# Performance work log

Measured on AMD Instinct MI355X. Metric: run time of the kernel, lower is better.

Reference implementation:

```python
import jax, jax.numpy as jnp
import numpy as np

HIDDEN = 2048
N_HEADS = 32
N_KV_HEADS = 8
HEAD_DIM = 64
ROPE_THETA = 500000.0
B, S = 1, 2048


def _rope_tables(seq_len):
    inv_freq = 1.0 / ROPE_THETA ** (jnp.arange(0, HEAD_DIM, 2, dtype=jnp.float32) / HEAD_DIM)
    angles = jnp.arange(seq_len, dtype=jnp.float32)[:, None] * inv_freq[None, :]
    return jnp.cos(angles), jnp.sin(angles)


def _apply_rope(x, cos, sin):
    # x: (B, S, H, D); cos/sin: (S, D//2)
    x1 = x[..., 0::2]
    x2 = x[..., 1::2]
    c = cos[None, :, None, :]
    s = sin[None, :, None, :]
    x1r = x1 * c - x2 * s
    x2r = x1 * s + x2 * c
    return jnp.stack([x1r, x2r], axis=-1).reshape(x.shape)


def setup_inputs() -> dict:
    key = jax.random.key(0)
    ks = jax.random.split(key, 5)
    hidden_states = jax.random.normal(ks[0], (B, S, HIDDEN), dtype=jnp.float32)
    # causal mask, broadcastable over (B, H, S, S)
    attention_mask = jnp.tril(jnp.ones((S, S), dtype=bool))[None, :, :]
    sc = 1.0 / np.sqrt(HIDDEN)
    wq = jax.random.normal(ks[1], (HIDDEN, N_HEADS * HEAD_DIM), dtype=jnp.float32) * sc
    wk = jax.random.normal(ks[2], (HIDDEN, N_KV_HEADS * HEAD_DIM), dtype=jnp.float32) * sc
    wv = jax.random.normal(ks[3], (HIDDEN, N_KV_HEADS * HEAD_DIM), dtype=jnp.float32) * sc
    wo = jax.random.normal(ks[4], (N_HEADS * HEAD_DIM, HIDDEN), dtype=jnp.float32) * sc
    return {"hidden_states": hidden_states, "attention_mask": attention_mask,
            "wq": wq, "wk": wk, "wv": wv, "wo": wo}


def reference(hidden_states, attention_mask, wq, wk, wv, wo):
    b, s, _ = hidden_states.shape
    groups = N_HEADS // N_KV_HEADS
    q = (hidden_states @ wq).reshape(b, s, N_HEADS, HEAD_DIM)
    k = (hidden_states @ wk).reshape(b, s, N_KV_HEADS, HEAD_DIM)
    v = (hidden_states @ wv).reshape(b, s, N_KV_HEADS, HEAD_DIM)
    cos, sin = _rope_tables(s)
    q = _apply_rope(q, cos, sin)
    k = _apply_rope(k, cos, sin)
    k = jnp.repeat(k, groups, axis=2)  # (b, s, H, D)
    v = jnp.repeat(v, groups, axis=2)
    q = q.transpose(0, 2, 1, 3)  # (b, H, s, D)
    k = k.transpose(0, 2, 1, 3)
    v = v.transpose(0, 2, 1, 3)
    scores = jnp.einsum('bhqd,bhkd->bhqk', q, k) / jnp.sqrt(jnp.float32(HEAD_DIM))
    scores = jnp.where(attention_mask[:, None, :, :], scores, -jnp.inf)
    probs = jax.nn.softmax(scores, axis=-1)
    out = jnp.einsum('bhqk,bhkd->bhqd', probs, v)
    out = out.transpose(0, 2, 1, 3).reshape(b, s, N_HEADS * HEAD_DIM)
    return out @ wo
```

## Files before the change

kernel.cpp:

```cpp
#include <hip/hip_runtime.h>

typedef __attribute__((ext_vector_type(8))) short short8;
typedef __attribute__((ext_vector_type(4))) float float4v;

union U4S8 { uint4 u; short8 s; };

__device__ __forceinline__ float bf2f(ushort u) {
    union { uint i; float f; } v; v.i = ((uint)u) << 16; return v.f;
}
__device__ __forceinline__ ushort f2bf(float f) {
    union { uint i; float f; } v; v.f = f;
    return (ushort)((v.i + 0x7FFFu + ((v.i >> 16) & 1u)) >> 16);
}
#if __has_builtin(__builtin_amdgcn_cvt_pk_bf16_f32)
__device__ __forceinline__ uint f2bf_pk(float a, float b) {
    auto r = __builtin_amdgcn_cvt_pk_bf16_f32(a, b);
    return __builtin_bit_cast(uint, r);
}
#else
__device__ __forceinline__ uint f2bf_pk(float a, float b) {
    return (uint)f2bf(a) | ((uint)f2bf(b) << 16);
}
#endif
__device__ __forceinline__ void gld_lds16(const ushort* g, ushort* l) {
    __builtin_amdgcn_global_load_lds((const __attribute__((address_space(1))) unsigned int*)g,
                                     (__attribute__((address_space(3))) unsigned int*)l,
                                     16, 0, 0);
}

__device__ __forceinline__ void tconv_body(const float* in, ushort* out,
                                           int C, int r0, int c0, int tid) {
    __shared__ float t[64][65];
    const int lrow = tid >> 2;
    const int lc   = (tid & 3) * 16;
    const float* ip = in + (size_t)(r0 + lrow) * C + c0 + lc;
#pragma unroll
    for (int i = 0; i < 4; i++) {
        float4 v = *(const float4*)(ip + 4 * i);
        t[lrow][lc + 4 * i + 0] = v.x; t[lrow][lc + 4 * i + 1] = v.y;
        t[lrow][lc + 4 * i + 2] = v.z; t[lrow][lc + 4 * i + 3] = v.w;
    }
    __syncthreads();
    ushort* op = out + (size_t)(c0 + lrow) * 2048 + r0 + lc;
#pragma unroll
    for (int i = 0; i < 8; i++)
        ((uint*)op)[i] = f2bf_pk(t[lc + 2 * i][lrow], t[lc + 2 * i + 1][lrow]);
}

__global__ __launch_bounds__(256) void prep(const float* __restrict__ hidden,
                                            const float* __restrict__ wq,
                                            const float* __restrict__ wk,
                                            const float* __restrict__ wv,
                                            ushort* __restrict__ hid,
                                            ushort* __restrict__ wT) {
    const int bx = blockIdx.x;
    if (bx < 2048) {
        const size_t i = ((size_t)bx * 256 + threadIdx.x) * 8;
        float4 a = *(const float4*)(hidden + i);
        float4 b = *(const float4*)(hidden + i + 4);
        uint4 u;
        u.x = f2bf_pk(a.x, a.y); u.y = f2bf_pk(a.z, a.w);
        u.z = f2bf_pk(b.x, b.y); u.w = f2bf_pk(b.z, b.w);
        *(uint4*)(hid + i) = u;
    } else {
        const int i = bx - 2048;
        const int xx = i % 48, yy = i / 48;
        const float* in; ushort* op; int C, cx;
        if (xx < 32)      { in = wq; op = wT;                        C = 2048; cx = xx; }
        else if (xx < 40) { in = wk; op = wT + (size_t)2048 * 2048;  C = 512;  cx = xx - 32; }
        else              { in = wv; op = wT + (size_t)2560 * 2048;  C = 512;  cx = xx - 40; }
        tconv_body(in, op, C, yy * 64, cx * 64, threadIdx.x);
    }
}

__global__ __launch_bounds__(256) void mid(ushort* __restrict__ Qb,
                                           ushort* __restrict__ Kc,
                                           const float* __restrict__ wo,
                                           ushort* __restrict__ woT) {
    const int bx = blockIdx.x;
    if (bx < 10240) {
        const int idx = bx * 256 + threadIdx.x;
        const int QP = 2048 * 1024;
        int s, p; ushort* base; float osc;
        if (idx < QP) { s = idx >> 10; p = idx & 1023; base = Qb; osc = 0.18033688f; }
        else { int r = idx - QP; s = r >> 8; p = r & 255; base = Kc; osc = 1.0f; }
        const int j = p & 31;
        float inv = __expf(-(float)(2 * j) * (1.0f / 64.0f) * 13.122363377404328f);
        float sn, c;
        sincosf((float)s * inv, &sn, &c);
        uint* p2 = (uint*)(base + (size_t)s * 3072 + 2 * p);
        uint xv = *p2;
        float x1 = bf2f((ushort)(xv & 0xFFFFu)), x2 = bf2f((ushort)(xv >> 16));
        *p2 = f2bf_pk((x1 * c - x2 * sn) * osc, (x1 * sn + x2 * c) * osc);
    } else {
        const int i = bx - 10240;
        tconv_body(wo, woT, 2048, (i >> 5) * 64, (i & 31) * 64, threadIdx.x);
    }
}

template <bool BF16OUT>
__global__ __launch_bounds__(256) void gemm_n64(const ushort* __restrict__ A,
                                                const ushort* __restrict__ Bt,
                                                void* __restrict__ Cout,
                                                int N, int K, int lda) {
    __shared__ ushort As[2][128 * 32];
    __shared__ ushort Bs[2][64 * 32];

    const int tid = threadIdx.x, w = tid >> 6, lane = tid & 63;
    const int lr = lane & 15, quad = lane >> 4;
    const int m0 = blockIdx.x * 128, n0 = blockIdx.y * 64;

    const int srow = lane >> 2;
    const int skb  = (lane & 3) ^ ((srow >> 1) & 3);

    const ushort* Ap = A  + (size_t)(m0 + srow) * lda + skb * 8;
    const ushort* Bp = Bt + (size_t)(n0 + w * 16 + srow) * K + skb * 8;

    float4v acc[2][4];
#pragma unroll
    for (int a = 0; a < 2; a++)
#pragma unroll
        for (int b = 0; b < 4; b++) { acc[a][b][0] = 0.f; acc[a][b][1] = 0.f; acc[a][b][2] = 0.f; acc[a][b][3] = 0.f; }

    const int fsw = (lr >> 1) & 3;

#pragma unroll
    for (int i = 0; i < 2; i++) {
        const int rt = 2 * w + i;
        gld_lds16(Ap + (size_t)(rt * 16) * lda, &As[0][rt * 512]);
    }
    gld_lds16(Bp, &Bs[0][w * 512]);

    const int niter = K >> 5;
    for (int it = 0; it < niter; it++) {
        const int b = it & 1;

        asm volatile("s_waitcnt vmcnt(0) lgkmcnt(0)\n\ts_barrier" ::: "memory");

        if (it + 1 < niter) {
            const int k1 = (it + 1) << 5;
#pragma unroll
            for (int i = 0; i < 2; i++) {
                const int rt = 2 * w + i;
                gld_lds16(Ap + (size_t)(rt * 16) * lda + k1, &As[1 - b][rt * 512]);
            }
            gld_lds16(Bp + k1, &Bs[1 - b][w * 512]);
        }

        short8 af[2], bf[4];
#pragma unroll
        for (int mt = 0; mt < 2; mt++)
            af[mt] = *(const short8*)&As[b][(w * 32 + mt * 16 + lr) * 32 + (quad ^ fsw) * 8];
#pragma unroll
        for (int nt = 0; nt < 4; nt++)
            bf[nt] = *(const short8*)&Bs[b][(nt * 16 + lr) * 32 + (quad ^ fsw) * 8];
#pragma unroll
        for (int mt = 0; mt < 2; mt++)
#pragma unroll
            for (int nt = 0; nt < 4; nt++)
                acc[mt][nt] = __builtin_amdgcn_mfma_f32_16x16x32_bf16(af[mt], bf[nt], acc[mt][nt], 0, 0, 0);
    }

    const int rbase = m0 + w * 32 + quad * 4;
    const int cbase = n0 + lr;
#pragma unroll
    for (int mt = 0; mt < 2; mt++)
#pragma unroll
        for (int nt = 0; nt < 4; nt++)
#pragma unroll
            for (int r = 0; r < 4; r++) {
                const size_t idx = (size_t)(rbase + mt * 16 + r) * N + cbase + nt * 16;
                if (BF16OUT) ((ushort*)Cout)[idx] = f2bf(acc[mt][nt][r]);
                else         ((float*)Cout)[idx]  = acc[mt][nt][r];
            }
}

__global__ __launch_bounds__(256) void attn_mfma(const ushort* __restrict__ Q,
                                                 const ushort* __restrict__ Kc,
                                                 const ushort* __restrict__ Vc,
                                                 ushort* __restrict__ O0,
                                                 ushort* __restrict__ O1,
                                                 float* __restrict__ L0,
                                                 float* __restrict__ L1) {
    __shared__ ushort Ks[2][64 * 64];
    __shared__ ushort Vt[2][64 * 64];
    __shared__ ushort Ps[4][16 * 64];

    const int tid = threadIdx.x, w = tid >> 6, lane = tid & 63;
    const int lr = lane & 15, quad = lane >> 4;
    const int h = blockIdx.y, g = h >> 2, z = blockIdx.z;

    const int dg = tid & 15;
    const int kl = tid >> 4;
    const int ksub = lane >> 3, dsub = lane & 7;
    ushort* Pw = Ps[w];
    ushort* Op = z ? O1 : O0;
    float*  Lp = z ? L1 : L0;

    const ushort* Vp0 = Vc + g * 64 + dg * 4 + (size_t)3072 * kl;
    const ushort* Kp0 = Kc + g * 64 + ((dsub ^ ksub) * 8) + (size_t)3072 * ksub;

    short8 onesf;
#pragma unroll
    for (int j = 0; j < 8; j++) onesf[j] = (short)0x3F80;

    for (int ti = 0; ti < 2; ti++) {
        const int bx = ti ? 31 - (int)blockIdx.x : (int)blockIdx.x;
        const int nch = (bx >= z) ? ((bx - z) >> 1) + 1 : 0;
        const int last = z + 2 * (nch - 1);

        const ushort* qp = Q + (size_t)(bx * 64 + w * 16 + lr) * 3072 + h * 64 + quad * 8;
        const short8 qf0 = *(const short8*)qp;
        const short8 qf1 = *(const short8*)(qp + 32);

        float4v oacc[4], lacc;
#pragma unroll
        for (int t = 0; t < 4; t++) { oacc[t][0] = 0.f; oacc[t][1] = 0.f; oacc[t][2] = 0.f; oacc[t][3] = 0.f; }
        lacc[0] = 0.f; lacc[1] = 0.f; lacc[2] = 0.f; lacc[3] = 0.f;

        uint2 vv[4];
        if (nch) {
#pragma unroll
            for (int t = 0; t < 4; t++)
                vv[t] = *(const uint2*)(Vp0 + (size_t)(z * 64 + 16 * t) * 3072);
        }
        __syncthreads();
        if (nch) {
#pragma unroll
            for (int i = 0; i < 2; i++) {
                const int rt = 2 * w + i;
                gld_lds16(Kp0 + (size_t)(z * 64 + rt * 8) * 3072, &Ks[0][rt * 512]);
            }
        }

        for (int c = 0; c < nch; c++) {
            const int kb = z + 2 * c;
            const int b = c & 1;
            ushort* bKs = Ks[b];
            ushort* bVt = Vt[b];

#pragma unroll
            for (int i = 0; i < 4; i++) {
                const uint sel = (i & 1) ? 0x07060302u : 0x05040100u;
                uint s0 = (i < 2) ? vv[0].x : vv[0].y;
                uint s1 = (i < 2) ? vv[1].x : vv[1].y;
                uint s2 = (i < 2) ? vv[2].x : vv[2].y;
                uint s3 = (i < 2) ? vv[3].x : vv[3].y;
                uint2 pk;
                pk.x = __builtin_amdgcn_perm(s1, s0, sel);
                pk.y = __builtin_amdgcn_perm(s3, s2, sel);
                *(uint2*)&bVt[(dg * 4 + i) * 64 + (kl ^ ((dg & 3) * 4 + i)) * 4] = pk;
            }

            const int kn = (c + 1 < nch) ? kb + 2 : last;
#pragma unroll
            for (int t = 0; t < 4; t++)
                vv[t] = *(const uint2*)(Vp0 + (size_t)(kn * 64 + 16 * t) * 3072);

            asm volatile("s_waitcnt vmcnt(4) lgkmcnt(0)\n\ts_barrier" ::: "memory");

#pragma unroll
            for (int i = 0; i < 2; i++) {
                const int rt = 2 * w + i;
                gld_lds16(Kp0 + (size_t)(kn * 64 + rt * 8) * 3072, &Ks[1 - b][rt * 512]);
            }

            float4v sacc[4];
#pragma unroll
            for (int t = 0; t < 4; t++) { sacc[t][0] = 0.f; sacc[t][1] = 0.f; sacc[t][2] = 0.f; sacc[t][3] = 0.f; }
#pragma unroll
            for (int t = 0; t < 4; t++) {
                const int krow = t * 16 + lr;
                const int sw = lr & 7;
                short8 kf0 = *(const short8*)&bKs[krow * 64 + ((quad)     ^ sw) * 8];
                short8 kf1 = *(const short8*)&bKs[krow * 64 + ((quad + 4) ^ sw) * 8];
                sacc[t] = __builtin_amdgcn_mfma_f32_16x16x32_bf16(qf0, kf0, sacc[t], 0, 0, 0);
                sacc[t] = __builtin_amdgcn_mfma_f32_16x16x32_bf16(qf1, kf1, sacc[t], 0, 0, 0);
            }

            if (kb == bx) {
#pragma unroll
                for (int r = 0; r < 4; r++) {
                    const int qr = w * 16 + quad * 4 + r;
                    float p0 = exp2f(sacc[0][r]), p1 = exp2f(sacc[1][r]);
                    float p2 = exp2f(sacc[2][r]), p3 = exp2f(sacc[3][r]);
                    if (lr > qr)      p0 = 0.f;
                    if (16 + lr > qr) p1 = 0.f;
                    if (32 + lr > qr) p2 = 0.f;
                    if (48 + lr > qr) p3 = 0.f;
                    const int prow = quad * 4 + r;
                    uint2 pk; pk.x = f2bf_pk(p0, p1); pk.y = f2bf_pk(p2, p3);
                    *(uint2*)&Pw[prow * 64 + (lr ^ prow) * 4] = pk;
                }
            } else {
#pragma unroll
                for (int r = 0; r < 4; r++) {
                    const int prow = quad * 4 + r;
                    uint2 pk;
                    pk.x = f2bf_pk(exp2f(sacc[0][r]), exp2f(sacc[1][r]));
                    pk.y = f2bf_pk(exp2f(sacc[2][r]), exp2f(sacc[3][r]));
                    *(uint2*)&Pw[prow * 64 + (lr ^ prow) * 4] = pk;
                }
            }

#pragma unroll
            for (int ks2 = 0; ks2 < 2; ks2++) {
                const int ub = ks2 * 8 + quad * 2;
                U4S8 pu;
                uint2 plo = *(const uint2*)&Pw[lr * 64 + ((ub)     ^ lr) * 4];
                uint2 phi = *(const uint2*)&Pw[lr * 64 + ((ub + 1) ^ lr) * 4];
                pu.u.x = plo.x; pu.u.y = plo.y; pu.u.z = phi.x; pu.u.w = phi.y;
                lacc = __builtin_amdgcn_mfma_f32_16x16x32_bf16(pu.s, onesf, lacc, 0, 0, 0);
#pragma unroll
                for (int t = 0; t < 4; t++) {
                    const int d = t * 16 + lr;
                    U4S8 vu;
                    uint2 vlo = *(const uint2*)&bVt[d * 64 + ((ub)     ^ lr) * 4];
                    uint2 vhi = *(const uint2*)&bVt[d * 64 + ((ub + 1) ^ lr) * 4];
                    vu.u.x = vlo.x; vu.u.y = vlo.y; vu.u.z = vhi.x; vu.u.w = vhi.y;
                    oacc[t] = __builtin_amdgcn_mfma_f32_16x16x32_bf16(pu.s, vu.s, oacc[t], 0, 0, 0);
                }
            }
        }

        ushort* op = Op + (size_t)(bx * 64 + w * 16 + quad * 4) * 2048 + h * 64 + lr;
#pragma unroll
        for (int t = 0; t < 4; t++)
#pragma unroll
            for (int r = 0; r < 4; r++)
                op[(size_t)r * 2048 + t * 16] = f2bf(oacc[t][r]);
        if (lr == 0) {
#pragma unroll
            for (int r = 0; r < 4; r++)
                Lp[h * 2048 + bx * 64 + w * 16 + quad * 4 + r] = lacc[r];
        }
    }
}

__global__ __launch_bounds__(256) void combine(const ushort* __restrict__ O0,
                                               const ushort* __restrict__ O1,
                                               const float* __restrict__ L0,
                                               const float* __restrict__ L1,
                                               ushort* __restrict__ Ab) {
    const int idx = blockIdx.x * 256 + threadIdx.x;
    const int r = idx >> 8;
    const int c8 = (idx & 255) * 8;
    const int h = c8 >> 6;
    const float rl = 1.0f / (L0[h * 2048 + r] + L1[h * 2048 + r]);
    uint4 a = *(const uint4*)(O0 + (size_t)r * 2048 + c8);
    uint4 b = *(const uint4*)(O1 + (size_t)r * 2048 + c8);
    uint ua[4] = {a.x, a.y, a.z, a.w}, ub[4] = {b.x, b.y, b.z, b.w};
    uint4 res;
    uint rr[4];
#pragma unroll
    for (int k = 0; k < 4; k++) {
        float x0 = bf2f((ushort)(ua[k] & 0xFFFFu)) + bf2f((ushort)(ub[k] & 0xFFFFu));
        float x1 = bf2f((ushort)(ua[k] >> 16))     + bf2f((ushort)(ub[k] >> 16));
        rr[k] = f2bf_pk(x0 * rl, x1 * rl);
    }
    res.x = rr[0]; res.y = rr[1]; res.z = rr[2]; res.w = rr[3];
    *(uint4*)(Ab + (size_t)r * 3072 + c8) = res;
}

extern "C" void kernel_launch(void* const* d_in, const int* in_sizes, int n_in,
                              void* d_out, int out_size, void* d_ws, size_t ws_size,
                              hipStream_t stream) {
    const float* hidden = (const float*)d_in[0];
    const float* wq = (const float*)d_in[2];
    const float* wk = (const float*)d_in[3];
    const float* wv = (const float*)d_in[4];
    const float* wo = (const float*)d_in[5];

    ushort* ws = (ushort*)d_ws;
    ushort* hid  = ws;
    ushort* wT   = ws + 4194304;
    ushort* QKV  = ws + 10485760;
    ushort* Qb = QKV;
    ushort* Kc = QKV + 2048;
    ushort* Vc = QKV + 2560;
    ushort* O1 = (ushort*)d_out;
    float*  L0 = (float*)((ushort*)d_out + 4194304);
    float*  L1 = L0 + 65536;

    prep<<<3584, 256, 0, stream>>>(hidden, wq, wk, wv, hid, wT);
    gemm_n64<true><<<dim3(16, 48), 256, 0, stream>>>(hid, wT, QKV, 3072, 2048, 2048);
    mid<<<11264, 256, 0, stream>>>(Qb, Kc, wo, wT);
    attn_mfma<<<dim3(16, 32, 2), 256, 0, stream>>>(Qb, Kc, Vc, hid , O1, L0, L1);
    combine<<<2048, 256, 0, stream>>>(hid, O1, L0, L1, Qb );
    gemm_n64<false><<<dim3(16, 32), 256, 0, stream>>>(Qb, wT, d_out, 2048, 2048, 3072);
}
```

Measured before the change: 243.3 us.

## Split-K both projection GEMMs into two halves and fold partial sums downstream

Both GEMMs are launched with a K-split of two along blockIdx.z, doubling the block count (768→1536 and 512→1024) so more CUs have work. For the QKV GEMM the second partial is written as bf16 into the output buffer, and the mid kernel adds the two partials before applying RoPE, with a new block range handling V. For the output GEMM, z=0 writes fp32 and a new addp kernel adds the bf16 second partial. This costs extra partial-buffer traffic, one extra launch, and rounding of the partial sums to bf16.

```diff
diff --git a/kernel.cpp b/kernel.cpp
--- a/kernel.cpp
+++ b/kernel.cpp
@@ -73,48 +73,66 @@
     }
 }
 
-__global__ __launch_bounds__(256) void mid(ushort* __restrict__ Qb,
-                                           ushort* __restrict__ Kc,
+__global__ __launch_bounds__(256) void mid(ushort* __restrict__ P0,
+                                           const ushort* __restrict__ P1,
                                            const float* __restrict__ wo,
                                            ushort* __restrict__ woT) {
     const int bx = blockIdx.x;
     if (bx < 10240) {
         const int idx = bx * 256 + threadIdx.x;
         const int QP = 2048 * 1024;
-        int s, p; ushort* base; float osc;
-        if (idx < QP) { s = idx >> 10; p = idx & 1023; base = Qb; osc = 0.18033688f; }
-        else { int r = idx - QP; s = r >> 8; p = r & 255; base = Kc; osc = 1.0f; }
+        int s, p; size_t off; float osc;
+        if (idx < QP) { s = idx >> 10; p = idx & 1023; off = (size_t)s * 3072 + 2 * p;        osc = 0.18033688f; }
+        else { int r = idx - QP; s = r >> 8; p = r & 255; off = (size_t)s * 3072 + 2048 + 2 * p; osc = 1.0f; }
         const int j = p & 31;
         float inv = __expf(-(float)(2 * j) * (1.0f / 64.0f) * 13.122363377404328f);
         float sn, c;
         sincosf((float)s * inv, &sn, &c);
-        uint* p2 = (uint*)(base + (size_t)s * 3072 + 2 * p);
-        uint xv = *p2;
-        float x1 = bf2f((ushort)(xv & 0xFFFFu)), x2 = bf2f((ushort)(xv >> 16));
-        *p2 = f2bf_pk((x1 * c - x2 * sn) * osc, (x1 * sn + x2 * c) * osc);
+        uint a = *(const uint*)(P0 + off);
+        uint b = *(const uint*)(P1 + off);
+        float x1 = bf2f((ushort)(a & 0xFFFFu)) + bf2f((ushort)(b & 0xFFFFu));
+        float x2 = bf2f((ushort)(a >> 16))     + bf2f((ushort)(b >> 16));
+        *(uint*)(P0 + off) = f2bf_pk((x1 * c - x2 * sn) * osc, (x1 * sn + x2 * c) * osc);
+    } else if (bx < 10752) {
+        const int e = (bx - 10240) * 256 + threadIdx.x;
+        const size_t off = (size_t)(e >> 6) * 3072 + 2560 + (e & 63) * 8;
+        uint4 a = *(const uint4*)(P0 + off);
+        uint4 b = *(const uint4*)(P1 + off);
+        uint ua[4] = {a.x, a.y, a.z, a.w}, ub[4] = {b.x, b.y, b.z, b.w};
+        uint rr[4];
+#pragma unroll
+        for (int k = 0; k < 4; k++) {
+            float lo = bf2f((ushort)(ua[k] & 0xFFFFu)) + bf2f((ushort)(ub[k] & 0xFFFFu));
+            float hi = bf2f((ushort)(ua[k] >> 16))     + bf2f((ushort)(ub[k] >> 16));
+            rr[k] = f2bf_pk(lo, hi);
+        }
+        uint4 res; res.x = rr[0]; res.y = rr[1]; res.z = rr[2]; res.w = rr[3];
+        *(uint4*)(P0 + off) = res;
     } else {
-        const int i = bx - 10240;
+        const int i = bx - 10752;
         tconv_body(wo, woT, 2048, (i >> 5) * 64, (i & 31) * 64, threadIdx.x);
     }
 }
 
-template <bool BF16OUT>
 __global__ __launch_bounds__(256) void gemm_n64(const ushort* __restrict__ A,
                                                 const ushort* __restrict__ Bt,
-                                                void* __restrict__ Cout,
-                                                int N, int K, int lda) {
+                                                ushort* __restrict__ Cb0,
+                                                ushort* __restrict__ Cb1,
+                                                float* __restrict__ Cf,
+                                                int N, int Kfull, int lda, int ksz) {
     __shared__ ushort As[2][128 * 32];
     __shared__ ushort Bs[2][64 * 32];
 
     const int tid = threadIdx.x, w = tid >> 6, lane = tid & 63;
     const int lr = lane & 15, quad = lane >> 4;
     const int m0 = blockIdx.x * 128, n0 = blockIdx.y * 64;
+    const int z = blockIdx.z, kb = z * ksz;
 
     const int srow = lane >> 2;
     const int skb  = (lane & 3) ^ ((srow >> 1) & 3);
 
-    const ushort* Ap = A  + (size_t)(m0 + srow) * lda + skb * 8;
-    const ushort* Bp = Bt + (size_t)(n0 + w * 16 + srow) * K + skb * 8;
+    const ushort* Ap = A  + (size_t)(m0 + srow) * lda + kb + skb * 8;
+    const ushort* Bp = Bt + (size_t)(n0 + w * 16 + srow) * Kfull + kb + skb * 8;
 
     float4v acc[2][4];
 #pragma unroll
@@ -131,7 +149,7 @@
     }
     gld_lds16(Bp, &Bs[0][w * 512]);
 
-    const int niter = K >> 5;
+    const int niter = ksz >> 5;
     for (int it = 0; it < niter; it++) {
         const int b = it & 1;
 
@@ -163,16 +181,24 @@
 
     const int rbase = m0 + w * 32 + quad * 4;
     const int cbase = n0 + lr;
-#pragma unroll
-    for (int mt = 0; mt < 2; mt++)
-#pragma unroll
-        for (int nt = 0; nt < 4; nt++)
-#pragma unroll
-            for (int r = 0; r < 4; r++) {
-                const size_t idx = (size_t)(rbase + mt * 16 + r) * N + cbase + nt * 16;
-                if (BF16OUT) ((ushort*)Cout)[idx] = f2bf(acc[mt][nt][r]);
-                else         ((float*)Cout)[idx]  = acc[mt][nt][r];
-            }
+    if (Cf && z == 0) {
+#pragma unroll
+        for (int mt = 0; mt < 2; mt++)
+#pragma unroll
+            for (int nt = 0; nt < 4; nt++)
+#pragma unroll
+                for (int r = 0; r < 4; r++)
+                    Cf[(size_t)(rbase + mt * 16 + r) * N + cbase + nt * 16] = acc[mt][nt][r];
+    } else {
+        ushort* Cb = z ? Cb1 : Cb0;
+#pragma unroll
+        for (int mt = 0; mt < 2; mt++)
+#pragma unroll
+            for (int nt = 0; nt < 4; nt++)
+#pragma unroll
+                for (int r = 0; r < 4; r++)
+                    Cb[(size_t)(rbase + mt * 16 + r) * N + cbase + nt * 16] = f2bf(acc[mt][nt][r]);
+    }
 }
 
 __global__ __launch_bounds__(256) void attn_mfma(const ushort* __restrict__ Q,
@@ -350,7 +376,6 @@
     uint4 a = *(const uint4*)(O0 + (size_t)r * 2048 + c8);
     uint4 b = *(const uint4*)(O1 + (size_t)r * 2048 + c8);
     uint ua[4] = {a.x, a.y, a.z, a.w}, ub[4] = {b.x, b.y, b.z, b.w};
-    uint4 res;
     uint rr[4];
 #pragma unroll
     for (int k = 0; k < 4; k++) {
@@ -358,8 +383,22 @@
         float x1 = bf2f((ushort)(ua[k] >> 16))     + bf2f((ushort)(ub[k] >> 16));
         rr[k] = f2bf_pk(x0 * rl, x1 * rl);
     }
-    res.x = rr[0]; res.y = rr[1]; res.z = rr[2]; res.w = rr[3];
+    uint4 res; res.x = rr[0]; res.y = rr[1]; res.z = rr[2]; res.w = rr[3];
     *(uint4*)(Ab + (size_t)r * 3072 + c8) = res;
+}
+
+__global__ __launch_bounds__(256) void addp(float* __restrict__ out,
+                                            const ushort* __restrict__ P1) {
+    const size_t i = ((size_t)blockIdx.x * 256 + threadIdx.x) * 8;
+    float4 a0 = *(const float4*)(out + i);
+    float4 a1 = *(const float4*)(out + i + 4);
+    uint4 b = *(const uint4*)(P1 + i);
+    a0.x += bf2f((ushort)(b.x & 0xFFFFu)); a0.y += bf2f((ushort)(b.x >> 16));
+    a0.z += bf2f((ushort)(b.y & 0xFFFFu)); a0.w += bf2f((ushort)(b.y >> 16));
+    a1.x += bf2f((ushort)(b.z & 0xFFFFu)); a1.y += bf2f((ushort)(b.z >> 16));
+    a1.z += bf2f((ushort)(b.w & 0xFFFFu)); a1.w += bf2f((ushort)(b.w >> 16));
+    *(float4*)(out + i)     = a0;
+    *(float4*)(out + i + 4) = a1;
 }
 
 extern "C" void kernel_launch(void* const* d_in, const int* in_sizes, int n_in,
@@ -378,14 +417,18 @@
     ushort* Qb = QKV;
     ushort* Kc = QKV + 2048;
     ushort* Vc = QKV + 2560;
-    ushort* O1 = (ushort*)d_out;
-    float*  L0 = (float*)((ushort*)d_out + 4194304);
-    float*  L1 = L0 + 65536;
+    ushort* QP1 = (ushort*)d_out;
+    ushort* O1  = (ushort*)d_out;
+    float*  L0  = (float*)((ushort*)d_out + 4194304);
+    float*  L1  = L0 + 65536;
 
     prep<<<3584, 256, 0, stream>>>(hidden, wq, wk, wv, hid, wT);
-    gemm_n64<true><<<dim3(16, 48), 256, 0, stream>>>(hid, wT, QKV, 3072, 2048, 2048);
-    mid<<<11264, 256, 0, stream>>>(Qb, Kc, wo, wT);
+    gemm_n64<<<dim3(16, 48, 2), 256, 0, stream>>>(hid, wT, QKV, QP1, nullptr,
+                                                  3072, 2048, 2048, 1024);
+    mid<<<11776, 256, 0, stream>>>(QKV, QP1, wo, wT);
     attn_mfma<<<dim3(16, 32, 2), 256, 0, stream>>>(Qb, Kc, Vc, hid , O1, L0, L1);
     combine<<<2048, 256, 0, stream>>>(hid, O1, L0, L1, Qb );
-    gemm_n64<false><<<dim3(16, 32), 256, 0, stream>>>(Qb, wT, d_out, 2048, 2048, 3072);
-}
+    gemm_n64<<<dim3(16, 32, 2), 256, 0, stream>>>(Qb, wT, nullptr, hid, (float*)d_out,
+                                                  2048, 2048, 3072, 1024);
+    addp<<<2048, 256, 0, stream>>>((float*)d_out, hid);
+}
```

New measurement: 250.2 us. +2.9%, slower.

## Fuse RoPE into QKV GEMM epilogue and move wo transpose into prep

Applied to the files above, without the earlier changes.

Applies rotary embedding (and the Q softmax scale) inside the QKV GEMM epilogue, exchanging pair partners with a lane shuffle. This removes the separate mid kernel that re-read and re-wrote Q and K. The wo transpose moves into the prep kernel, and buffers are remapped so combine writes in place and the output projection reads hid directly. The cost is extra sincos work per GEMM output element and a reshuffled workspace/output aliasing scheme.

```diff
diff --git a/kernel.cpp b/kernel.cpp
--- a/kernel.cpp
+++ b/kernel.cpp
@@ -51,8 +51,10 @@
                                             const float* __restrict__ wq,
                                             const float* __restrict__ wk,
                                             const float* __restrict__ wv,
+                                            const float* __restrict__ wo,
                                             ushort* __restrict__ hid,
-                                            ushort* __restrict__ wT) {
+                                            ushort* __restrict__ wT,
+                                            ushort* __restrict__ woT) {
     const int bx = blockIdx.x;
     if (bx < 2048) {
         const size_t i = ((size_t)bx * 256 + threadIdx.x) * 8;
@@ -62,7 +64,7 @@
         u.x = f2bf_pk(a.x, a.y); u.y = f2bf_pk(a.z, a.w);
         u.z = f2bf_pk(b.x, b.y); u.w = f2bf_pk(b.z, b.w);
         *(uint4*)(hid + i) = u;
-    } else {
+    } else if (bx < 3584) {
         const int i = bx - 2048;
         const int xx = i % 48, yy = i / 48;
         const float* in; ushort* op; int C, cx;
@@ -70,30 +72,8 @@
         else if (xx < 40) { in = wk; op = wT + (size_t)2048 * 2048;  C = 512;  cx = xx - 32; }
         else              { in = wv; op = wT + (size_t)2560 * 2048;  C = 512;  cx = xx - 40; }
         tconv_body(in, op, C, yy * 64, cx * 64, threadIdx.x);
-    }
-}
-
-__global__ __launch_bounds__(256) void mid(ushort* __restrict__ Qb,
-                                           ushort* __restrict__ Kc,
-                                           const float* __restrict__ wo,
-                                           ushort* __restrict__ woT) {
-    const int bx = blockIdx.x;
-    if (bx < 10240) {
-        const int idx = bx * 256 + threadIdx.x;
-        const int QP = 2048 * 1024;
-        int s, p; ushort* base; float osc;
-        if (idx < QP) { s = idx >> 10; p = idx & 1023; base = Qb; osc = 0.18033688f; }
-        else { int r = idx - QP; s = r >> 8; p = r & 255; base = Kc; osc = 1.0f; }
-        const int j = p & 31;
-        float inv = __expf(-(float)(2 * j) * (1.0f / 64.0f) * 13.122363377404328f);
-        float sn, c;
-        sincosf((float)s * inv, &sn, &c);
-        uint* p2 = (uint*)(base + (size_t)s * 3072 + 2 * p);
-        uint xv = *p2;
-        float x1 = bf2f((ushort)(xv & 0xFFFFu)), x2 = bf2f((ushort)(xv >> 16));
-        *p2 = f2bf_pk((x1 * c - x2 * sn) * osc, (x1 * sn + x2 * c) * osc);
     } else {
-        const int i = bx - 10240;
+        const int i = bx - 3584;
         tconv_body(wo, woT, 2048, (i >> 5) * 64, (i & 31) * 64, threadIdx.x);
     }
 }
@@ -102,7 +82,7 @@
 __global__ __launch_bounds__(256) void gemm_n64(const ushort* __restrict__ A,
                                                 const ushort* __restrict__ Bt,
                                                 void* __restrict__ Cout,
-                                                int N, int K, int lda) {
+                                                int N, int K, int lda, int ropeQKV) {
     __shared__ ushort As[2][128 * 32];
     __shared__ ushort Bs[2][64 * 32];
 
@@ -163,16 +143,47 @@
 
     const int rbase = m0 + w * 32 + quad * 4;
     const int cbase = n0 + lr;
-#pragma unroll
-    for (int mt = 0; mt < 2; mt++)
-#pragma unroll
-        for (int nt = 0; nt < 4; nt++)
-#pragma unroll
-            for (int r = 0; r < 4; r++) {
-                const size_t idx = (size_t)(rbase + mt * 16 + r) * N + cbase + nt * 16;
-                if (BF16OUT) ((ushort*)Cout)[idx] = f2bf(acc[mt][nt][r]);
-                else         ((float*)Cout)[idx]  = acc[mt][nt][r];
-            }
+    if (BF16OUT) {
+        ushort* Cb = (ushort*)Cout;
+        if (ropeQKV && (int)blockIdx.y < 40) {
+            const float osc = ((int)blockIdx.y < 32) ? 0.18033688f : 1.0f;
+            const float sgn = (lr & 1) ? 1.0f : -1.0f;
+#pragma unroll
+            for (int nt = 0; nt < 4; nt++) {
+                const int col = cbase + nt * 16;
+                const int j = (col >> 1) & 31;
+                const float inv = __expf(-(float)(2 * j) * (1.0f / 64.0f) * 13.122363377404328f);
+#pragma unroll
+                for (int mt = 0; mt < 2; mt++)
+#pragma unroll
+                    for (int r = 0; r < 4; r++) {
+                        const int row = rbase + mt * 16 + r;
+                        float sn, cs;
+                        sincosf((float)row * inv, &sn, &cs);
+                        const float mine = acc[mt][nt][r];
+                        const float partner = __shfl_xor(mine, 1);
+                        Cb[(size_t)row * N + col] = f2bf((mine * cs + sgn * partner * sn) * osc);
+                    }
+            }
+        } else {
+#pragma unroll
+            for (int mt = 0; mt < 2; mt++)
+#pragma unroll
+                for (int nt = 0; nt < 4; nt++)
+#pragma unroll
+                    for (int r = 0; r < 4; r++)
+                        Cb[(size_t)(rbase + mt * 16 + r) * N + cbase + nt * 16] = f2bf(acc[mt][nt][r]);
+        }
+    } else {
+        float* Cf = (float*)Cout;
+#pragma unroll
+        for (int mt = 0; mt < 2; mt++)
+#pragma unroll
+            for (int nt = 0; nt < 4; nt++)
+#pragma unroll
+                for (int r = 0; r < 4; r++)
+                    Cf[(size_t)(rbase + mt * 16 + r) * N + cbase + nt * 16] = acc[mt][nt][r];
+    }
 }
 
 __global__ __launch_bounds__(256) void attn_mfma(const ushort* __restrict__ Q,
@@ -337,11 +348,10 @@
     }
 }
 
-__global__ __launch_bounds__(256) void combine(const ushort* __restrict__ O0,
+__global__ __launch_bounds__(256) void combine(ushort* __restrict__ O0,
                                                const ushort* __restrict__ O1,
                                                const float* __restrict__ L0,
-                                               const float* __restrict__ L1,
-                                               ushort* __restrict__ Ab) {
+                                               const float* __restrict__ L1) {
     const int idx = blockIdx.x * 256 + threadIdx.x;
     const int r = idx >> 8;
     const int c8 = (idx & 255) * 8;
@@ -350,7 +360,6 @@
     uint4 a = *(const uint4*)(O0 + (size_t)r * 2048 + c8);
     uint4 b = *(const uint4*)(O1 + (size_t)r * 2048 + c8);
     uint ua[4] = {a.x, a.y, a.z, a.w}, ub[4] = {b.x, b.y, b.z, b.w};
-    uint4 res;
     uint rr[4];
 #pragma unroll
     for (int k = 0; k < 4; k++) {
@@ -358,8 +367,8 @@
         float x1 = bf2f((ushort)(ua[k] >> 16))     + bf2f((ushort)(ub[k] >> 16));
         rr[k] = f2bf_pk(x0 * rl, x1 * rl);
     }
-    res.x = rr[0]; res.y = rr[1]; res.z = rr[2]; res.w = rr[3];
-    *(uint4*)(Ab + (size_t)r * 3072 + c8) = res;
+    uint4 res; res.x = rr[0]; res.y = rr[1]; res.z = rr[2]; res.w = rr[3];
+    *(uint4*)(O0 + (size_t)r * 2048 + c8) = res;
 }
 
 extern "C" void kernel_launch(void* const* d_in, const int* in_sizes, int n_in,
@@ -372,20 +381,18 @@
     const float* wo = (const float*)d_in[5];
 
     ushort* ws = (ushort*)d_ws;
-    ushort* hid  = ws;
-    ushort* wT   = ws + 4194304;
-    ushort* QKV  = ws + 10485760;
-    ushort* Qb = QKV;
-    ushort* Kc = QKV + 2048;
-    ushort* Vc = QKV + 2560;
-    ushort* O1 = (ushort*)d_out;
-    float*  L0 = (float*)((ushort*)d_out + 4194304);
-    float*  L1 = L0 + 65536;
-
-    prep<<<3584, 256, 0, stream>>>(hidden, wq, wk, wv, hid, wT);
-    gemm_n64<true><<<dim3(16, 48), 256, 0, stream>>>(hid, wT, QKV, 3072, 2048, 2048);
-    mid<<<11264, 256, 0, stream>>>(Qb, Kc, wo, wT);
-    attn_mfma<<<dim3(16, 32, 2), 256, 0, stream>>>(Qb, Kc, Vc, hid , O1, L0, L1);
-    combine<<<2048, 256, 0, stream>>>(hid, O1, L0, L1, Qb );
-    gemm_n64<false><<<dim3(16, 32), 256, 0, stream>>>(Qb, wT, d_out, 2048, 2048, 3072);
-}
+    ushort* hid = ws;
+    ushort* wT  = ws + 4194304;
+    ushort* woT = ws + 10485760;
+    ushort* O1  = wT;
+    float*  L0  = (float*)(ws + 8388608);
+    float*  L1  = L0 + 65536;
+    ushort* QKV = (ushort*)d_out;
+
+    prep<<<4608, 256, 0, stream>>>(hidden, wq, wk, wv, wo, hid, wT, woT);
+    gemm_n64<true><<<dim3(16, 48), 256, 0, stream>>>(hid, wT, QKV, 3072, 2048, 2048, 1);
+    attn_mfma<<<dim3(16, 32, 2), 256, 0, stream>>>(QKV, QKV + 2048, QKV + 2560,
+                                                   hid , O1, L0, L1);
+    combine<<<2048, 256, 0, stream>>>(hid, O1, L0, L1);
+    gemm_n64<false><<<dim3(16, 32), 256, 0, stream>>>(hid, woT, d_out, 2048, 2048, 2048, 0);
+}
```

Result: faster. 236.6 us (-2.7%).
